# Optimization experiments

Hardware: AMD Instinct MI355X
Metric: run time of the kernel (lower is better)

## Reference

```python
import jax, jax.numpy as jnp
import numpy as np

D = 1024; H = 8; QLR = 384; KVLR = 256; NOPE = 128; ROPE = 64; VD = 128
E = 8; TOPK = 2; INTER = 512; NSH = 2; B = 2; T = 2048
QKD = NOPE + ROPE  # 192


def _rms(x, w, eps=1e-6):
    return x * jax.lax.rsqrt(jnp.mean(x * x, axis=-1, keepdims=True) + eps) * w


def _rope(x, cos, sin):
    # x: [B,T,h,ROPE]; pairs are consecutive elements (torch view(...,-1,2)).
    x0 = x[..., 0::2]
    x1 = x[..., 1::2]
    c = cos[None, :, None, :]
    s = sin[None, :, None, :]
    y0 = x0 * c - x1 * s
    y1 = x0 * s + x1 * c
    return jnp.stack([y0, y1], axis=-1).reshape(x.shape)


def setup_inputs() -> dict:
    key = jax.random.key(0)
    ks = jax.random.split(key, 12)
    def w(k, shape, scale=0.02):
        return jax.random.normal(k, shape, dtype=jnp.float32) * scale
    inv = 1.0 / (10000.0 ** (jnp.arange(0, ROPE, 2, dtype=jnp.float32) / ROPE))
    ang = jnp.arange(T, dtype=jnp.float32)[:, None] * inv[None, :]  # [T, ROPE//2]
    return {
        "x": jax.random.normal(ks[0], (B, T, D), dtype=jnp.float32),
        "freqs_cos": jnp.cos(ang),
        "freqs_sin": jnp.sin(ang),
        "rmsn1_w": jnp.ones((D,), jnp.float32),
        "rmsn2_w": jnp.ones((D,), jnp.float32),
        "latent_w": w(ks[1], (D, QLR + KVLR + ROPE)),
        "q_norm_w": jnp.ones((QLR,), jnp.float32),
        "q_up_w": w(ks[2], (QLR, H * QKD)),
        "kv_norm_w": jnp.ones((KVLR,), jnp.float32),
        "kv_up_w": w(ks[3], (KVLR, H * (NOPE + VD))),
        "c_proj_w": w(ks[4], (D, D)),
        "gate_w": w(ks[5], (D, E)),
        "sh_w1": w(ks[6], (D, INTER * NSH)),
        "sh_w2": w(ks[7], (INTER * NSH, D)),
        "sh_w3": w(ks[8], (D, INTER * NSH)),
        "e_w1": w(ks[9], (E, D, INTER)),
        "e_w2": w(ks[10], (E, INTER, D)),
        "e_w3": w(ks[11], (E, D, INTER)),
    }


def reference(x, freqs_cos, freqs_sin, rmsn1_w, rmsn2_w, latent_w, q_norm_w,
              q_up_w, kv_norm_w, kv_up_w, c_proj_w, gate_w, sh_w1, sh_w2,
              sh_w3, e_w1, e_w2, e_w3):
    Bx, Tx, _ = x.shape
    # ---- MLA attention ----
    h = _rms(x, rmsn1_w)
    lat = h @ latent_w
    q_l, kv_l, k_r = jnp.split(lat, [QLR, QLR + KVLR], axis=-1)
    q = (_rms(q_l, q_norm_w) @ q_up_w).reshape(Bx, Tx, H, QKD)
    q_n, q_r = q[..., :NOPE], q[..., NOPE:]
    q_r = _rope(q_r, freqs_cos, freqs_sin)
    q = jnp.concatenate([q_n, q_r], axis=-1)  # [B,T,H,QKD]
    kv = (_rms(kv_l, kv_norm_w) @ kv_up_w).reshape(Bx, Tx, H, NOPE + VD)
    k_n, v = kv[..., :NOPE], kv[..., NOPE:]
    k_r = _rope(k_r[:, :, None, :], freqs_cos, freqs_sin)
    k_r = jnp.broadcast_to(k_r, (Bx, Tx, H, ROPE))
    k = jnp.concatenate([k_n, k_r], axis=-1)
    scale = 1.0 / jnp.sqrt(jnp.float32(QKD))
    scores = jnp.einsum('bqhd,bkhd->bhqk', q, k) * scale
    causal = jnp.tril(jnp.ones((Tx, Tx), dtype=bool))
    scores = jnp.where(causal, scores, jnp.finfo(scores.dtype).min)
    attn = jax.nn.softmax(scores, axis=-1)
    y = jnp.einsum('bhqk,bkhd->bqhd', attn, v).reshape(Bx, Tx, D)
    x = x + y @ c_proj_w
    # ---- DeepSeekMoE ----
    h2 = _rms(x, rmsn2_w).reshape(-1, D)  # [N, D]
    y_sh = (jax.nn.silu(h2 @ sh_w1) * (h2 @ sh_w3)) @ sh_w2
    scores_g = jax.nn.softmax(h2 @ gate_w, axis=-1)  # [N, E]
    w_top, idx = jax.lax.top_k(scores_g, TOPK)  # weights == gathered original scores
    # combine weights per expert (route_scale = 1.0)
    cw = jnp.sum(jax.nn.one_hot(idx, E, dtype=h2.dtype) * w_top[..., None], axis=1)  # [N, E]
    h1 = jnp.einsum('nd,edi->eni', h2, e_w1)
    h3 = jnp.einsum('nd,edi->eni', h2, e_w3)
    out_e = jnp.einsum('eni,eid->end', jax.nn.silu(h1) * h3, e_w2)  # [E, N, D]
    y_moe = y_sh + jnp.einsum('end,ne->nd', out_e, cw)
    return x + y_moe.reshape(Bx, Tx, D)
```

## Files before the change

### kernel.cpp

```cpp
#include <hip/hip_runtime.h>
#include <hip/hip_bf16.h>
#include <math.h>

#define D_ 1024
#define H_ 8
#define QLR_ 384
#define KVLR_ 256
#define NOPE_ 128
#define ROPE_ 64
#define VD_ 128
#define E_ 8
#define INTER_ 512
#define B_ 2
#define T_ 2048
#define QKD_ 192
#define NTOK (B_*T_)
#define LSTR 4608
#define MAXMB 72

typedef __attribute__((ext_vector_type(8))) short short8;
typedef __attribute__((ext_vector_type(4))) float f32x4;
typedef __attribute__((ext_vector_type(4))) unsigned short us4;

__device__ __forceinline__ unsigned short f2bf(float f) {
  union { float f; unsigned u; } v; v.f = f;
  return (unsigned short)((v.u + 0x7FFFu + ((v.u >> 16) & 1u)) >> 16);
}
__device__ __forceinline__ float bf2f(unsigned short h) {
  union { unsigned u; float f; } v; v.u = ((unsigned)h) << 16;
  return v.f;
}

#define GLD16(SRC, DST) __builtin_amdgcn_global_load_lds( \
    (__attribute__((address_space(1))) void*)(SRC), \
    (__attribute__((address_space(3))) void*)(DST), 16, 0, 0)

#define DPPF(v, ctrl) __int_as_float(__builtin_amdgcn_update_dpp(0, __float_as_int(v), ctrl, 0xF, 0xF, true))
__device__ __forceinline__ float dppmax16(float v) {
  v = fmaxf(v, DPPF(v, 0xB1));
  v = fmaxf(v, DPPF(v, 0x4E));
  v = fmaxf(v, DPPF(v, 0x124));
  v = fmaxf(v, DPPF(v, 0x128));
  return v;
}
__device__ __forceinline__ float dppsum16(float v) {
  v += DPPF(v, 0xB1);
  v += DPPF(v, 0x4E);
  v += DPPF(v, 0x124);
  v += DPPF(v, 0x128);
  return v;
}

__device__ __forceinline__ void trans32(const float* __restrict__ src, unsigned short* __restrict__ dst,
                                        int R, int C, int c0, int r0, float (*tile)[33]) {
  int tx = threadIdx.x & 31, ty = threadIdx.x >> 5;
  #pragma unroll
  for (int i = 0; i < 4; ++i) {
    int rr = ty + i * 8;
    tile[rr][tx] = src[(size_t)(r0 + rr) * C + c0 + tx];
  }
  __syncthreads();
  #pragma unroll
  for (int i = 0; i < 4; ++i) {
    int rr = ty + i * 8;
    dst[(size_t)(c0 + rr) * R + r0 + tx] = f2bf(tile[tx][rr]);
  }
}
__device__ __forceinline__ void trans32p(const float* __restrict__ src, unsigned short* __restrict__ dst,
                                         int K, int C1, int c0, int r0, int f, float (*tile)[33]) {
  int tx = threadIdx.x & 31, ty = threadIdx.x >> 5;
  #pragma unroll
  for (int i = 0; i < 4; ++i) {
    int rr = ty + i * 8;
    tile[rr][tx] = src[(size_t)(r0 + rr) * C1 + c0 + tx];
  }
  __syncthreads();
  #pragma unroll
  for (int i = 0; i < 4; ++i) {
    int cc = ty + i * 8;
    int c = c0 + cc;
    int n = ((c >> 4) << 5) + (c & 15) + f;
    dst[(size_t)n * K + r0 + tx] = f2bf(tile[tx][cc]);
  }
}

__global__ __launch_bounds__(256) void prep1(
    const float* __restrict__ x, const float* __restrict__ rw, unsigned short* __restrict__ h_bf,
    const float* __restrict__ latent_w, unsigned short* __restrict__ Wlat) {
  __shared__ float tile[32][33];
  int b = blockIdx.x;
  if (b < NTOK) {
    int tid = threadIdx.x;
    const float* xr = x + (size_t)b * D_;
    float v[4]; float ss = 0.f;
    #pragma unroll
    for (int j = 0; j < 4; ++j) { v[j] = xr[tid + j * 256]; ss += v[j] * v[j]; }
    for (int o = 1; o < 64; o <<= 1) ss += __shfl_xor(ss, o);
    if ((tid & 63) == 0) tile[32][tid >> 6] = ss;
    __syncthreads();
    float inv = 1.f / sqrtf((tile[32][0] + tile[32][1] + tile[32][2] + tile[32][3]) / D_ + 1e-6f);
    #pragma unroll
    for (int j = 0; j < 4; ++j) {
      int i = tid + j * 256;
      h_bf[(size_t)b * D_ + i] = f2bf(v[j] * inv * rw[i]);
    }
    return;
  }
  b -= NTOK;
  trans32(latent_w, Wlat, 1024, 704, (b % 22) * 32, (b / 22) * 32, tile);
}

__global__ __launch_bounds__(256) void prep2(
    const unsigned short* __restrict__ h_bf, const unsigned short* __restrict__ Wlat,
    unsigned short* __restrict__ lat,
    const float* __restrict__ q_up_w, unsigned short* __restrict__ Wqup,
    const float* __restrict__ kv_up_w, unsigned short* __restrict__ Wkv,
    const float* __restrict__ c_proj_w, unsigned short* __restrict__ Wcp,
    const float* __restrict__ sh_w1, const float* __restrict__ sh_w3, unsigned short* __restrict__ Wsh13,
    const float* __restrict__ sh_w2, unsigned short* __restrict__ Wsh2,
    const float* __restrict__ e_w1, const float* __restrict__ e_w3, unsigned short* __restrict__ Wew13,
    const float* __restrict__ e_w2, unsigned short* __restrict__ Wew2) {
  __shared__ __align__(16) unsigned short As[128 * 32];
  __shared__ __align__(16) unsigned short Bs[128 * 32];
  __shared__ float tile[32][33];
  int b = blockIdx.x;
  if (b < 192) {
    const int tid = threadIdx.x, lane = tid & 63, wave = tid >> 6;
    const int wm = wave >> 1, wn = wave & 1;
    const int bm = (b / 6) * 128, bn = (b % 6) * 128;
    const int r = lane & 15, g = lane >> 4;
    f32x4 acc[4][4];
    #pragma unroll
    for (int i = 0; i < 4; ++i)
      #pragma unroll
      for (int j = 0; j < 4; ++j) acc[i][j] = (f32x4)0.f;
    const int rl0 = wave * 16 + (lane >> 2), rl1 = rl0 + 64;
    const int kc = (lane & 3) * 8;
    char* AsB = (char*)As; char* BsB = (char*)Bs;
    for (int k0 = 0; k0 < 1024; k0 += 32) {
      GLD16(h_bf + (size_t)(bm + rl0) * 1024 + k0 + kc, AsB + wave * 1024);
      GLD16(h_bf + (size_t)(bm + rl1) * 1024 + k0 + kc, AsB + (wave + 4) * 1024);
      GLD16(Wlat + (size_t)(bn + rl0) * 1024 + k0 + kc, BsB + wave * 1024);
      GLD16(Wlat + (size_t)(bn + rl1) * 1024 + k0 + kc, BsB + (wave + 4) * 1024);
      __syncthreads();
      short8 af[4], bfr[4];
      #pragma unroll
      for (int mi = 0; mi < 4; ++mi)
        af[mi] = *(const short8*)(As + (wm * 64 + mi * 16 + r) * 32 + g * 8);
      #pragma unroll
      for (int nj = 0; nj < 4; ++nj)
        bfr[nj] = *(const short8*)(Bs + (wn * 64 + nj * 16 + r) * 32 + g * 8);
      #pragma unroll
      for (int mi = 0; mi < 4; ++mi)
        #pragma unroll
        for (int nj = 0; nj < 4; ++nj)
          acc[mi][nj] = __builtin_amdgcn_mfma_f32_16x16x32_bf16(af[mi], bfr[nj], acc[mi][nj], 0, 0, 0);
      __syncthreads();
    }
    const int orow0 = wm * 64 + g * 4;
    const int ocol0 = bn + wn * 64 + r;
    #pragma unroll
    for (int mi = 0; mi < 4; ++mi)
      #pragma unroll
      for (int reg = 0; reg < 4; ++reg) {
        int mrow = bm + orow0 + mi * 16 + reg;
        size_t bas = (size_t)mrow * 768 + ocol0;
        #pragma unroll
        for (int nj = 0; nj < 4; ++nj) lat[bas + nj * 16] = f2bf(acc[mi][nj][reg]);
      }
    return;
  }
  b -= 192;
  if (b < 576) { trans32(q_up_w, Wqup, 384, 1536, (b % 48) * 32, (b / 48) * 32, tile); return; }
  b -= 576;
  if (b < 512) { trans32(kv_up_w, Wkv, 256, 2048, (b % 64) * 32, (b / 64) * 32, tile); return; }
  b -= 512;
  if (b < 1024) { trans32(c_proj_w, Wcp, 1024, 1024, (b % 32) * 32, (b / 32) * 32, tile); return; }
  b -= 1024;
  if (b < 1024) { trans32(sh_w2, Wsh2, 1024, 1024, (b % 32) * 32, (b / 32) * 32, tile); return; }
  b -= 1024;
  if (b < 2048) {
    int z = b / 1024, idx = b % 1024;
    trans32p(z ? sh_w3 : sh_w1, Wsh13, 1024, 1024, (idx % 32) * 32, (idx / 32) * 32, z * 16, tile);
    return;
  }
  b -= 2048;
  if (b < 8192) {
    int z = b / 512, idx = b % 512;
    int bat = z >> 1, f = (z & 1) * 16;
    const float* src = ((z & 1) ? e_w3 : e_w1) + (size_t)bat * 1024 * 512;
    trans32p(src, Wew13 + (size_t)bat * 1024 * 1024, 1024, 512, (idx % 16) * 32, (idx / 16) * 32, f, tile);
    return;
  }
  b -= 8192;
  {
    int z = b / 512, idx = b % 512;
    trans32(e_w2 + (size_t)z * 512 * 1024, Wew2 + (size_t)z * 1024 * 512,
            512, 1024, (idx % 32) * 32, (idx / 32) * 32, tile);
  }
}

__global__ __launch_bounds__(256) void lat_post(
    const unsigned short* __restrict__ lat, const float* __restrict__ qw,
    const float* __restrict__ kw, const float* __restrict__ fc, const float* __restrict__ fs,
    unsigned short* __restrict__ qn, unsigned short* __restrict__ kvn,
    unsigned short* __restrict__ kr) {
  int row = blockIdx.x, tid = threadIdx.x;
  int lane = tid & 63, wv = tid >> 6;
  const unsigned short* lr = lat + (size_t)row * 768;
  float s1 = 0.f, s2 = 0.f;
  for (int i = tid; i < QLR_; i += 256) { float v = bf2f(lr[i]); s1 += v * v; }
  { float v = bf2f(lr[QLR_ + tid]); s2 = v * v; }
  for (int o = 1; o < 64; o <<= 1) { s1 += __shfl_xor(s1, o); s2 += __shfl_xor(s2, o); }
  __shared__ float red[8];
  if (lane == 0) { red[wv] = s1; red[4 + wv] = s2; }
  __syncthreads();
  float inv1 = 1.f / sqrtf((red[0] + red[1] + red[2] + red[3]) / QLR_ + 1e-6f);
  float inv2 = 1.f / sqrtf((red[4] + red[5] + red[6] + red[7]) / KVLR_ + 1e-6f);
  for (int i = tid; i < QLR_; i += 256)
    qn[(size_t)row * QLR_ + i] = f2bf(bf2f(lr[i]) * inv1 * qw[i]);
  kvn[(size_t)row * KVLR_ + tid] = f2bf(bf2f(lr[QLR_ + tid]) * inv2 * kw[tid]);
  if (tid < 32) {
    int t = row & (T_ - 1);
    float c = fc[t * 32 + tid], s = fs[t * 32 + tid];
    float x0 = bf2f(lr[640 + 2 * tid]), x1 = bf2f(lr[640 + 2 * tid + 1]);
    kr[(size_t)row * ROPE_ + 2 * tid]     = f2bf(x0 * c - x1 * s);
    kr[(size_t)row * ROPE_ + 2 * tid + 1] = f2bf(x0 * s + x1 * c);
  }
}

template<int MODE>
__global__ __launch_bounds__(256) void gemm_bf16(
    const unsigned short* __restrict__ A, const unsigned short* __restrict__ Bt,
    void* __restrict__ Cv, int M, int N, int K,
    const float* __restrict__ addv) {
  __shared__ __align__(16) unsigned short As[128 * 32];
  __shared__ __align__(16) unsigned short Bs[128 * 32];
  const int tid = threadIdx.x;
  const int lane = tid & 63, wave = tid >> 6;
  const int wm = wave >> 1, wn = wave & 1;
  const int bm = blockIdx.y * 128, bn = blockIdx.x * 128;
  const int r = lane & 15, g = lane >> 4;

  f32x4 acc[4][4];
  #pragma unroll
  for (int i = 0; i < 4; ++i)
    #pragma unroll
    for (int j = 0; j < 4; ++j) acc[i][j] = (f32x4)0.f;

  const int rl0 = wave * 16 + (lane >> 2);
  const int rl1 = rl0 + 64;
  const int kc = (lane & 3) * 8;
  char* AsB = (char*)As; char* BsB = (char*)Bs;

  for (int k0 = 0; k0 < K; k0 += 32) {
    GLD16(A + (size_t)(bm + rl0) * K + k0 + kc, AsB + wave * 1024);
    GLD16(A + (size_t)(bm + rl1) * K + k0 + kc, AsB + (wave + 4) * 1024);
    GLD16(Bt + (size_t)(bn + rl0) * K + k0 + kc, BsB + wave * 1024);
    GLD16(Bt + (size_t)(bn + rl1) * K + k0 + kc, BsB + (wave + 4) * 1024);
    __syncthreads();
    short8 af[4], bfr[4];
    #pragma unroll
    for (int mi = 0; mi < 4; ++mi)
      af[mi] = *(const short8*)(As + (wm * 64 + mi * 16 + r) * 32 + g * 8);
    #pragma unroll
    for (int nj = 0; nj < 4; ++nj)
      bfr[nj] = *(const short8*)(Bs + (wn * 64 + nj * 16 + r) * 32 + g * 8);
    #pragma unroll
    for (int mi = 0; mi < 4; ++mi)
      #pragma unroll
      for (int nj = 0; nj < 4; ++nj)
        acc[mi][nj] = __builtin_amdgcn_mfma_f32_16x16x32_bf16(af[mi], bfr[nj], acc[mi][nj], 0, 0, 0);
    __syncthreads();
  }

  const int orow0 = wm * 64 + g * 4;
  const int ocol0 = bn + wn * 64 + r;
  #pragma unroll
  for (int mi = 0; mi < 4; ++mi) {
    #pragma unroll
    for (int reg = 0; reg < 4; ++reg) {
      int mrow = bm + orow0 + mi * 16 + reg;
      size_t bas = (size_t)mrow * N + ocol0;
      if (MODE == 0) {
        unsigned short* C = (unsigned short*)Cv;
        #pragma unroll
        for (int nj = 0; nj < 4; ++nj) C[bas + nj * 16] = f2bf(acc[mi][nj][reg]);
      } else {
        float* C = (float*)Cv;
        #pragma unroll
        for (int nj = 0; nj < 4; ++nj) C[bas + nj * 16] = acc[mi][nj][reg] + addv[bas + nj * 16];
      }
    }
  }
}

__global__ __launch_bounds__(256) void gemm_qkv(
    const unsigned short* __restrict__ qn, const unsigned short* __restrict__ Wqup,
    const unsigned short* __restrict__ kvn, const unsigned short* __restrict__ Wkv,
    unsigned short* __restrict__ qq, unsigned short* __restrict__ kvb,
    unsigned short* __restrict__ vtg) {
  __shared__ __align__(16) unsigned short As[128 * 32];
  __shared__ __align__(16) unsigned short Bs[128 * 32];
  const int tid = threadIdx.x;
  const int lane = tid & 63, wave = tid >> 6;
  const int wm = wave >> 1, wn = wave & 1;
  const bool isQ = blockIdx.x < 12;
  const int bx = isQ ? blockIdx.x : blockIdx.x - 12;
  const unsigned short* A  = isQ ? qn : kvn;
  const unsigned short* Bt = isQ ? Wqup : Wkv;
  const int K = isQ ? QLR_ : KVLR_;
  const int bm = blockIdx.y * 128, bn = bx * 128;
  const int r = lane & 15, g = lane >> 4;

  f32x4 acc[4][4];
  #pragma unroll
  for (int i = 0; i < 4; ++i)
    #pragma unroll
    for (int j = 0; j < 4; ++j) acc[i][j] = (f32x4)0.f;

  const int rl0 = wave * 16 + (lane >> 2);
  const int rl1 = rl0 + 64;
  const int kc = (lane & 3) * 8;
  char* AsB = (char*)As; char* BsB = (char*)Bs;

  for (int k0 = 0; k0 < K; k0 += 32) {
    GLD16(A + (size_t)(bm + rl0) * K + k0 + kc, AsB + wave * 1024);
    GLD16(A + (size_t)(bm + rl1) * K + k0 + kc, AsB + (wave + 4) * 1024);
    GLD16(Bt + (size_t)(bn + rl0) * K + k0 + kc, BsB + wave * 1024);
    GLD16(Bt + (size_t)(bn + rl1) * K + k0 + kc, BsB + (wave + 4) * 1024);
    __syncthreads();
    short8 af[4], bfr[4];
    #pragma unroll
    for (int mi = 0; mi < 4; ++mi)
      af[mi] = *(const short8*)(As + (wm * 64 + mi * 16 + r) * 32 + g * 8);
    #pragma unroll
    for (int nj = 0; nj < 4; ++nj)
      bfr[nj] = *(const short8*)(Bs + (wn * 64 + nj * 16 + r) * 32 + g * 8);
    #pragma unroll
    for (int mi = 0; mi < 4; ++mi)
      #pragma unroll
      for (int nj = 0; nj < 4; ++nj)
        acc[mi][nj] = __builtin_amdgcn_mfma_f32_16x16x32_bf16(af[mi], bfr[nj], acc[mi][nj], 0, 0, 0);
    __syncthreads();
  }

  if (isQ) {
    const int orow0 = wm * 64 + g * 4;
    const int ocol0 = bn + wn * 64 + r;
    #pragma unroll
    for (int mi = 0; mi < 4; ++mi)
      #pragma unroll
      for (int reg = 0; reg < 4; ++reg) {
        int mrow = bm + orow0 + mi * 16 + reg;
        size_t bas = (size_t)mrow * 1536 + ocol0;
        #pragma unroll
        for (int nj = 0; nj < 4; ++nj) qq[bas + nj * 16] = f2bf(acc[mi][nj][reg]);
      }
  } else {
    const int colbase = bn + wn * 64;
    const int b = bm >> 11;
    const int hh = colbase >> 8;
    if ((colbase & 255) < 128) {
      #pragma unroll
      for (int mi = 0; mi < 4; ++mi)
        #pragma unroll
        for (int reg = 0; reg < 4; ++reg) {
          int mrow = bm + wm * 64 + mi * 16 + g * 4 + reg;
          size_t bas = (size_t)mrow * 2048 + colbase + r;
          #pragma unroll
          for (int nj = 0; nj < 4; ++nj) kvb[bas + nj * 16] = f2bf(acc[mi][nj][reg]);
        }
    } else {
      const int tl0 = (bm & 2047) + wm * 64 + g * 4;
      const int d0 = (colbase & 255) - 128 + r;
      const size_t bhbase = (size_t)(b * 8 + hh) * 64;
      #pragma unroll
      for (int mi = 0; mi < 4; ++mi) {
        int t = tl0 + mi * 16;
        size_t tb = (bhbase + (t >> 5)) * 4096 + (t & 31);
        #pragma unroll
        for (int nj = 0; nj < 4; ++nj) {
          int d = d0 + nj * 16;
          us4 pk;
          #pragma unroll
          for (int reg = 0; reg < 4; ++reg) pk[reg] = f2bf(acc[mi][nj][reg]);
          *(us4*)(vtg + tb + (size_t)d * 32) = pk;
        }
      }
    }
  }
}

__global__ __launch_bounds__(256) void gemm_ffn13(
    const unsigned short* __restrict__ h2b, const unsigned short* __restrict__ Wsh13,
    unsigned short* __restrict__ t1m,
    const unsigned short* __restrict__ Wew13, unsigned short* __restrict__ ehm,
    const int* __restrict__ lists, const int* __restrict__ map, const int* __restrict__ sbase) {
  __shared__ __align__(16) unsigned short As[128 * 32];
  __shared__ __align__(16) unsigned short Bs[128 * 32];
  const int i = blockIdx.x;
  const bool isSh = i < 512;
  const int tid = threadIdx.x, lane = tid & 63, wave = tid >> 6;
  const int wm = wave >> 1, wn = wave & 1;
  const int r = lane & 15, g = lane >> 4;
  const int rl0 = wave * 16 + (lane >> 2), rl1 = rl0 + 64;
  const int kc = (lane & 3) * 8;

  int bn, e = 0, ib = 0, bm = 0;
  const unsigned short* Bt;
  int ar0, ar1;
  const unsigned short* A;
  if (isSh) {
    bn = (i & 15) * 128; bm = (i >> 4) * 128;
    Bt = Wsh13; A = h2b;
    ar0 = bm + rl0; ar1 = bm + rl1;
  } else {
    int j = i - 512;
    bn = (j & 7) * 128;
    int mb = map[j >> 3];
    if (mb < 0) return;
    e = mb >> 16; ib = mb & 0xFFFF;
    Bt = Wew13 + (size_t)e * 1024 * 1024; A = h2b;
    ar0 = lists[e * LSTR + ib * 128 + rl0]; if (ar0 < 0) ar0 = 0;
    ar1 = lists[e * LSTR + ib * 128 + rl1]; if (ar1 < 0) ar1 = 0;
  }

  f32x4 acc[4][4];
  #pragma unroll
  for (int a = 0; a < 4; ++a)
    #pragma unroll
    for (int bj = 0; bj < 4; ++bj) acc[a][bj] = (f32x4)0.f;
  char* AsB = (char*)As; char* BsB = (char*)Bs;

  for (int k0 = 0; k0 < 1024; k0 += 32) {
    GLD16(A + (size_t)ar0 * 1024 + k0 + kc, AsB + wave * 1024);
    GLD16(A + (size_t)ar1 * 1024 + k0 + kc, AsB + (wave + 4) * 1024);
    GLD16(Bt + (size_t)(bn + rl0) * 1024 + k0 + kc, BsB + wave * 1024);
    GLD16(Bt + (size_t)(bn + rl1) * 1024 + k0 + kc, BsB + (wave + 4) * 1024);
    __syncthreads();
    short8 af[4], bfr[4];
    #pragma unroll
    for (int mi = 0; mi < 4; ++mi)
      af[mi] = *(const short8*)(As + (wm * 64 + mi * 16 + r) * 32 + g * 8);
    #pragma unroll
    for (int nj = 0; nj < 4; ++nj)
      bfr[nj] = *(const short8*)(Bs + (wn * 64 + nj * 16 + r) * 32 + g * 8);
    #pragma unroll
    for (int mi = 0; mi < 4; ++mi)
      #pragma unroll
      for (int nj = 0; nj < 4; ++nj)
        acc[mi][nj] = __builtin_amdgcn_mfma_f32_16x16x32_bf16(af[mi], bfr[nj], acc[mi][nj], 0, 0, 0);
    __syncthreads();
  }

  if (isSh) {
    const int hc = ((bn + wn * 64) >> 1) + r;
    #pragma unroll
    for (int mi = 0; mi < 4; ++mi)
      #pragma unroll
      for (int reg = 0; reg < 4; ++reg) {
        int mrow = bm + wm * 64 + mi * 16 + g * 4 + reg;
        #pragma unroll
        for (int p = 0; p < 2; ++p) {
          float a = acc[mi][2 * p][reg], b3 = acc[mi][2 * p + 1][reg];
          t1m[(size_t)mrow * 1024 + hc + p * 16] = f2bf((a / (1.f + __expf(-a))) * b3);
        }
      }
  } else {
    const int sb = sbase[e] + ib * 128;
    const int hc = ((bn + wn * 64) >> 1) + r;
    #pragma unroll
    for (int mi = 0; mi < 4; ++mi)
      #pragma unroll
      for (int reg = 0; reg < 4; ++reg) {
        int srow = sb + wm * 64 + mi * 16 + g * 4 + reg;
        #pragma unroll
        for (int p = 0; p < 2; ++p) {
          float a = acc[mi][2 * p][reg], b3 = acc[mi][2 * p + 1][reg];
          ehm[(size_t)srow * 512 + hc + p * 16] = f2bf((a / (1.f + __expf(-a))) * b3);
        }
      }
  }
}

__global__ __launch_bounds__(256) void gemm_ffn2(
    const unsigned short* __restrict__ t1m, const unsigned short* __restrict__ Wsh2,
    const unsigned short* __restrict__ ehm, const unsigned short* __restrict__ Wew2,
    float* __restrict__ out,
    const int* __restrict__ lists, const int* __restrict__ map, const int* __restrict__ sbase,
    const float* __restrict__ cw) {
  __shared__ __align__(16) unsigned short As[128 * 32];
  __shared__ __align__(16) unsigned short Bs[128 * 32];
  const int i = blockIdx.x;
  const bool isSh = i < 256;
  const int tid = threadIdx.x, lane = tid & 63, wave = tid >> 6;
  const int wm = wave >> 1, wn = wave & 1;
  const int r = lane & 15, g = lane >> 4;
  const int rl0 = wave * 16 + (lane >> 2), rl1 = rl0 + 64;
  const int kc = (lane & 3) * 8;

  int bn, e = 0, ib = 0, bm = 0, K;
  const unsigned short* A;
  const unsigned short* Bt;
  if (isSh) {
    bn = (i & 7) * 128; bm = (i >> 3) * 128;
    A = t1m; Bt = Wsh2; K = 1024;
  } else {
    int j = i - 256;
    bn = (j & 7) * 128;
    int mb = map[j >> 3];
    if (mb < 0) return;
    e = mb >> 16; ib = mb & 0xFFFF;
    bm = sbase[e] + ib * 128;
    A = ehm; Bt = Wew2 + (size_t)e * 512 * 1024; K = 512;
  }

  f32x4 acc[4][4];
  #pragma unroll
  for (int a = 0; a < 4; ++a)
    #pragma unroll
    for (int bj = 0; bj < 4; ++bj) acc[a][bj] = (f32x4)0.f;
  char* AsB = (char*)As; char* BsB = (char*)Bs;

  for (int k0 = 0; k0 < K; k0 += 32) {
    GLD16(A + (size_t)(bm + rl0) * K + k0 + kc, AsB + wave * 1024);
    GLD16(A + (size_t)(bm + rl1) * K + k0 + kc, AsB + (wave + 4) * 1024);
    GLD16(Bt + (size_t)(bn + rl0) * K + k0 + kc, BsB + wave * 1024);
    GLD16(Bt + (size_t)(bn + rl1) * K + k0 + kc, BsB + (wave + 4) * 1024);
    __syncthreads();
    short8 af[4], bfr[4];
    #pragma unroll
    for (int mi = 0; mi < 4; ++mi)
      af[mi] = *(const short8*)(As + (wm * 64 + mi * 16 + r) * 32 + g * 8);
    #pragma unroll
    for (int nj = 0; nj < 4; ++nj)
      bfr[nj] = *(const short8*)(Bs + (wn * 64 + nj * 16 + r) * 32 + g * 8);
    #pragma unroll
    for (int mi = 0; mi < 4; ++mi)
      #pragma unroll
      for (int nj = 0; nj < 4; ++nj)
        acc[mi][nj] = __builtin_amdgcn_mfma_f32_16x16x32_bf16(af[mi], bfr[nj], acc[mi][nj], 0, 0, 0);
    __syncthreads();
  }

  const int ocol0 = bn + wn * 64 + r;
  if (isSh) {
    #pragma unroll
    for (int mi = 0; mi < 4; ++mi)
      #pragma unroll
      for (int reg = 0; reg < 4; ++reg) {
        int mrow = bm + wm * 64 + mi * 16 + g * 4 + reg;
        #pragma unroll
        for (int nj = 0; nj < 4; ++nj)
          atomicAdd(out + (size_t)mrow * 1024 + ocol0 + nj * 16, acc[mi][nj][reg]);
      }
  } else {
    #pragma unroll
    for (int mi = 0; mi < 4; ++mi)
      #pragma unroll
      for (int reg = 0; reg < 4; ++reg) {
        int orow = wm * 64 + mi * 16 + g * 4 + reg;
        int tok = lists[e * LSTR + ib * 128 + orow];
        if (tok >= 0) {
          float wt = cw[(size_t)tok * E_ + e];
          #pragma unroll
          for (int nj = 0; nj < 4; ++nj)
            atomicAdd(out + (size_t)tok * 1024 + ocol0 + nj * 16, acc[mi][nj][reg] * wt);
        }
      }
  }
}

#define AQ 128
#define AK 32
#define VP 40
__global__ __launch_bounds__(512) void attn_mfma(
    const unsigned short* __restrict__ q,
    const unsigned short* __restrict__ kv,
    const unsigned short* __restrict__ kr,
    const unsigned short* __restrict__ vt,
    const float* __restrict__ fcos, const float* __restrict__ fsin,
    unsigned short* __restrict__ po,
    float* __restrict__ pml) {
  __shared__ __align__(16) unsigned short Ks[AK * 192];
  __shared__ __align__(16) unsigned short Vl[128 * VP];
  __shared__ __align__(16) unsigned short Ps[8 * 16 * VP];
  const int tid = threadIdx.x, lane = tid & 63, wave = tid >> 6;
  const int r = lane & 15, g = lane >> 4;
  const int bh = blockIdx.y, b = bh >> 3, h = bh & 7;
  const int qt = gridDim.x - 1 - blockIdx.x;
  const int q0 = qt * AQ;
  const int half = blockIdx.z;
  const int hnt = 2 * (qt + 1);
  const int kb = half * hnt, ke = kb + hnt;
  const size_t bT = (size_t)b * T_;
  const unsigned short* vbase = vt + (size_t)bh * 64 * 4096;
  char* KsB = (char*)Ks;

  short8 qf[6];
  const int qrow = q0 + wave * 16 + r;
  {
    const unsigned short* qb = q + ((bT + qrow) * H_ + h) * 192;
    #pragma unroll
    for (int kk = 0; kk < 6; ++kk) qf[kk] = *(const short8*)(qb + kk * 32 + g * 8);
    #pragma unroll
    for (int kk = 4; kk < 6; ++kk) {
      int i0 = (kk - 4) * 16 + g * 4;
      #pragma unroll
      for (int p = 0; p < 4; ++p) {
        float cc = fcos[qrow * 32 + i0 + p], sn = fsin[qrow * 32 + i0 + p];
        float x0 = bf2f((unsigned short)qf[kk][2 * p]), x1 = bf2f((unsigned short)qf[kk][2 * p + 1]);
        qf[kk][2 * p]     = (short)f2bf(x0 * cc - x1 * sn);
        qf[kk][2 * p + 1] = (short)f2bf(x0 * sn + x1 * cc);
      }
    }
  }

  float m_i[4], l_i[4];
  f32x4 o[8];
  #pragma unroll
  for (int i = 0; i < 4; ++i) { m_i[i] = -1e30f; l_i[i] = 0.f; }
  #pragma unroll
  for (int cb = 0; cb < 8; ++cb) o[cb] = (f32x4)0.f;

  const float scale2 = 0.07216878364870322f * 1.44269504088896f;

  const int kr0r = tid / 24, kr0c = tid % 24;
  const bool k1v = tid < 256;
  const int kr1r = (tid + 512) / 24, kr1c = (tid + 512) % 24;

  short8 kreg0, kreg1, vreg;
  {
    int kk0 = kb * AK;
    kreg0 = (kr0c < 16)
      ? *(const short8*)(kv + ((bT + kk0 + kr0r) * H_ + h) * 256 + kr0c * 8)
      : *(const short8*)(kr + (bT + kk0 + kr0r) * 64 + (kr0c - 16) * 8);
    if (k1v)
      kreg1 = (kr1c < 16)
        ? *(const short8*)(kv + ((bT + kk0 + kr1r) * H_ + h) * 256 + kr1c * 8)
        : *(const short8*)(kr + (bT + kk0 + kr1r) * 64 + (kr1c - 16) * 8);
    vreg = *(const short8*)(vbase + (size_t)kb * 4096 + tid * 8);
  }

  for (int kt = kb; kt < ke; ++kt) {
    __builtin_amdgcn_s_barrier();
    __builtin_amdgcn_sched_barrier(0);
    *(short8*)(KsB + ((kr0r * 384 + kr0c * 16) ^ ((kr0r & 7) << 4))) = kreg0;
    if (k1v)
      *(short8*)(KsB + ((kr1r * 384 + kr1c * 16) ^ ((kr1r & 7) << 4))) = kreg1;
    *(short8*)(Vl + (tid >> 2) * VP + (tid & 3) * 8) = vreg;
    asm volatile("s_waitcnt lgkmcnt(0)" ::: "memory");
    __builtin_amdgcn_s_barrier();
    __builtin_amdgcn_sched_barrier(0);

    if (kt + 1 < ke) {
      int k1 = (kt + 1) * AK;
      kreg0 = (kr0c < 16)
        ? *(const short8*)(kv + ((bT + k1 + kr0r) * H_ + h) * 256 + kr0c * 8)
        : *(const short8*)(kr + (bT + k1 + kr0r) * 64 + (kr0c - 16) * 8);
      if (k1v)
        kreg1 = (kr1c < 16)
          ? *(const short8*)(kv + ((bT + k1 + kr1r) * H_ + h) * 256 + kr1c * 8)
          : *(const short8*)(kr + (bT + k1 + kr1r) * 64 + (kr1c - 16) * 8);
      vreg = *(const short8*)(vbase + (size_t)(kt + 1) * 4096 + tid * 8);
    }

    const int k0 = kt * AK;
    f32x4 sf0 = (f32x4)0.f, sf1 = (f32x4)0.f;
    {
      int ksw = (r & 7) << 4;
      __builtin_amdgcn_s_setprio(1);
      #pragma unroll
      for (int kk = 0; kk < 6; ++kk) {
        short8 b0 = *(const short8*)(KsB + ((r * 384 + kk * 64 + g * 16) ^ ksw));
        short8 b1 = *(const short8*)(KsB + (((16 + r) * 384 + kk * 64 + g * 16) ^ ksw));
        sf0 = __builtin_amdgcn_mfma_f32_16x16x32_bf16(qf[kk], b0, sf0, 0, 0, 0);
        sf1 = __builtin_amdgcn_mfma_f32_16x16x32_bf16(qf[kk], b1, sf1, 0, 0, 0);
      }
      __builtin_amdgcn_s_setprio(0);
    }

    float fac[4];
    bool needs = false;
    const bool bnd = (k0 + AK > q0);
    #pragma unroll
    for (int reg = 0; reg < 4; ++reg) {
      float s0 = sf0[reg] * scale2;
      float s1 = sf1[reg] * scale2;
      if (bnd) {
        int qp = q0 + wave * 16 + g * 4 + reg;
        if (k0 + r > qp) s0 = -1e30f;
        if (k0 + 16 + r > qp) s1 = -1e30f;
      }
      float mt = dppmax16(fmaxf(s0, s1));
      float fc = 1.f, mn = m_i[reg];
      if (mt > mn + 8.f) {
        mn = mt; fc = exp2f(m_i[reg] - mn); m_i[reg] = mn; needs = true;
      }
      float e0 = exp2f(s0 - mn), e1 = exp2f(s1 - mn);
      float rs = dppsum16(e0 + e1);
      l_i[reg] = l_i[reg] * fc + rs;
      fac[reg] = fc;
      __hip_bfloat162 pk = __float22bfloat162_rn(float2{e0, e1});
      unsigned u = *(unsigned*)&pk;
      int prow = g * 4 + reg;
      Ps[wave * 16 * VP + prow * VP + r] = (unsigned short)u;
      Ps[wave * 16 * VP + prow * VP + 16 + r] = (unsigned short)(u >> 16);
    }
    if (__any(needs)) {
      #pragma unroll
      for (int cb = 0; cb < 8; ++cb)
        #pragma unroll
        for (int reg = 0; reg < 4; ++reg) o[cb][reg] *= fac[reg];
    }
    short8 pa = *(const short8*)(Ps + wave * 16 * VP + r * VP + g * 8);
    __builtin_amdgcn_s_setprio(1);
    #pragma unroll
    for (int cb = 0; cb < 8; ++cb) {
      short8 vb = *(const short8*)(Vl + (cb * 16 + r) * VP + g * 8);
      o[cb] = __builtin_amdgcn_mfma_f32_16x16x32_bf16(pa, vb, o[cb], 0, 0, 0);
    }
    __builtin_amdgcn_s_setprio(0);
  }

  const int slab = (bh * 16 + qt) * 2 + half;
  unsigned short* pob = po + (size_t)slab * 16384;
  float* pmlb = pml + (size_t)slab * 256;
  #pragma unroll
  for (int reg = 0; reg < 4; ++reg) {
    int row = wave * 16 + g * 4 + reg;
    if (r == 0) { pmlb[row * 2] = m_i[reg]; pmlb[row * 2 + 1] = l_i[reg]; }
    #pragma unroll
    for (int cb = 0; cb < 8; ++cb)
      pob[row * 128 + cb * 16 + r] = f2bf(o[cb][reg]);
  }
}

__global__ __launch_bounds__(512) void attn_combine(
    const unsigned short* __restrict__ po, const float* __restrict__ pml,
    unsigned short* __restrict__ y) {
  const int qt = blockIdx.x, bh = blockIdx.y, b = bh >> 3, h = bh & 7;
  const int s0 = (bh * 16 + qt) * 2, s1 = s0 + 1;
  const int row = threadIdx.x >> 2;
  const int qp = threadIdx.x & 3;
  float m0 = pml[(size_t)s0 * 256 + row * 2], l0 = pml[(size_t)s0 * 256 + row * 2 + 1];
  float m1 = pml[(size_t)s1 * 256 + row * 2], l1 = pml[(size_t)s1 * 256 + row * 2 + 1];
  float m = fmaxf(m0, m1);
  float e0 = exp2f(m0 - m), e1 = exp2f(m1 - m);
  float inv = 1.f / (l0 * e0 + l1 * e1);
  e0 *= inv; e1 *= inv;
  const unsigned short* o0 = po + (size_t)s0 * 16384 + row * 128 + qp * 32;
  const unsigned short* o1 = po + (size_t)s1 * 16384 + row * 128 + qp * 32;
  unsigned short* yb = y + ((size_t)(b * T_ + qt * 128 + row)) * 1024 + h * 128 + qp * 32;
  #pragma unroll
  for (int v = 0; v < 4; ++v) {
    short8 a = *(const short8*)(o0 + v * 8);
    short8 c = *(const short8*)(o1 + v * 8);
    short8 w;
    #pragma unroll
    for (int j = 0; j < 8; ++j)
      w[j] = (short)f2bf(bf2f((unsigned short)a[j]) * e0 + bf2f((unsigned short)c[j]) * e1);
    *(short8*)(yb + v * 8) = w;
  }
}

__global__ __launch_bounds__(256) void rms2_gate(
    const float* __restrict__ xo, const float* __restrict__ rw, const float* __restrict__ gw,
    unsigned short* __restrict__ h2b, float* __restrict__ cw) {
  int row = blockIdx.x, tid = threadIdx.x;
  int lane = tid & 63, wv = tid >> 6;
  const float* xr = xo + (size_t)row * D_;
  float v[4]; float ss = 0.f;
  #pragma unroll
  for (int j = 0; j < 4; ++j) { v[j] = xr[tid + j * 256]; ss += v[j] * v[j]; }
  for (int o = 1; o < 64; o <<= 1) ss += __shfl_xor(ss, o);
  __shared__ float red[4];
  if (lane == 0) red[wv] = ss;
  __syncthreads();
  float inv = 1.f / sqrtf((red[0] + red[1] + red[2] + red[3]) / D_ + 1e-6f);
  float a[E_] = {0, 0, 0, 0, 0, 0, 0, 0};
  #pragma unroll
  for (int j = 0; j < 4; ++j) {
    int i = tid + j * 256;
    float hv = v[j] * inv * rw[i];
    h2b[(size_t)row * D_ + i] = f2bf(hv);
    const float* wr = gw + (size_t)i * E_;
    #pragma unroll
    for (int e = 0; e < E_; ++e) a[e] += hv * wr[e];
  }
  #pragma unroll
  for (int e = 0; e < E_; ++e) {
    float t = a[e];
    for (int o = 1; o < 64; o <<= 1) t += __shfl_xor(t, o);
    a[e] = t;
  }
  __shared__ float ga[4][E_];
  if (lane == 0)
    #pragma unroll
    for (int e = 0; e < E_; ++e) ga[wv][e] = a[e];
  __syncthreads();
  if (tid == 0) {
    float lg[E_];
    #pragma unroll
    for (int e = 0; e < E_; ++e) lg[e] = ga[0][e] + ga[1][e] + ga[2][e] + ga[3][e];
    float mx = lg[0];
    #pragma unroll
    for (int e = 1; e < E_; ++e) mx = fmaxf(mx, lg[e]);
    float sum = 0.f; float p[E_];
    #pragma unroll
    for (int e = 0; e < E_; ++e) { p[e] = __expf(lg[e] - mx); sum += p[e]; }
    float is = 1.f / sum;
    int i1 = 0; float b1 = p[0];
    #pragma unroll
    for (int e = 1; e < E_; ++e) if (p[e] > b1) { b1 = p[e]; i1 = e; }
    int i2 = -1; float b2 = -1.f;
    #pragma unroll
    for (int e = 0; e < E_; ++e) if (e != i1 && p[e] > b2) { b2 = p[e]; i2 = e; }
    #pragma unroll
    for (int e = 0; e < E_; ++e)
      cw[(size_t)row * E_ + e] = (e == i1) ? b1 * is : (e == i2 ? b2 * is : 0.f);
  }
}

__global__ __launch_bounds__(256) void moe_build(const float* __restrict__ cw,
                                                 int* __restrict__ lists, int* __restrict__ counts) {
  int e = blockIdx.x, tid = threadIdx.x;
  int lane = tid & 63, wv = tid >> 6;
  __shared__ int wsum[4];
  __shared__ int base;
  if (tid == 0) base = 0;
  __syncthreads();
  for (int c0 = 0; c0 < NTOK; c0 += 256) {
    int tok = c0 + tid;
    bool f = cw[(size_t)tok * E_ + e] > 0.f;
    unsigned long long m = __ballot(f);
    int pos = __popcll(m & ((1ull << lane) - 1ull));
    if (lane == 0) wsum[wv] = __popcll(m);
    __syncthreads();
    int woff = base;
    #pragma unroll
    for (int w = 0; w < 4; ++w) if (w < wv) woff += wsum[w];
    if (f) lists[e * LSTR + woff + pos] = tok;
    __syncthreads();
    if (tid == 0) base += wsum[0] + wsum[1] + wsum[2] + wsum[3];
    __syncthreads();
  }
  int cnt = base;
  int padded = (cnt + 127) & ~127;
  for (int i2 = cnt + tid; i2 < padded; i2 += 256) lists[e * LSTR + i2] = -1;
  if (tid == 0) { counts[e] = cnt; counts[8 + e] = padded >> 7; }
}

__global__ void moe_finalize(const int* __restrict__ counts, int* __restrict__ map,
                             int* __restrict__ sbase) {
  if (threadIdx.x == 0 && blockIdx.x == 0) {
    int cum = 0;
    for (int e = 0; e < E_; ++e) {
      sbase[e] = cum * 128;
      int nb = counts[8 + e];
      for (int i = 0; i < nb; ++i) map[cum + i] = (e << 16) | i;
      cum += nb;
    }
    for (; cum < MAXMB; ++cum) map[cum] = -1;
  }
}

extern "C" void kernel_launch(void* const* d_in, const int* in_sizes, int n_in,
                              void* d_out, int out_size, void* d_ws, size_t ws_size,
                              hipStream_t stream) {
  const float* x        = (const float*)d_in[0];
  const float* fcos     = (const float*)d_in[1];
  const float* fsin     = (const float*)d_in[2];
  const float* rmsn1_w  = (const float*)d_in[3];
  const float* rmsn2_w  = (const float*)d_in[4];
  const float* latent_w = (const float*)d_in[5];
  const float* q_norm_w = (const float*)d_in[6];
  const float* q_up_w   = (const float*)d_in[7];
  const float* kv_norm_w= (const float*)d_in[8];
  const float* kv_up_w  = (const float*)d_in[9];
  const float* c_proj_w = (const float*)d_in[10];
  const float* gate_w   = (const float*)d_in[11];
  const float* sh_w1    = (const float*)d_in[12];
  const float* sh_w2    = (const float*)d_in[13];
  const float* sh_w3    = (const float*)d_in[14];
  const float* e_w1     = (const float*)d_in[15];
  const float* e_w2     = (const float*)d_in[16];
  const float* e_w3     = (const float*)d_in[17];
  float* out = (float*)d_out;

  char* base = (char*)d_ws;
  size_t off = 0;
  auto take = [&](size_t bytes) { char* p = base + off; off += (bytes + 255) & ~(size_t)255; return p; };
  unsigned short* Wlat  = (unsigned short*)take((size_t)768 * 1024 * 2);
  unsigned short* Wqup  = (unsigned short*)take((size_t)1536 * 384 * 2);
  unsigned short* Wkv   = (unsigned short*)take((size_t)2048 * 256 * 2);
  unsigned short* Wcp   = (unsigned short*)take((size_t)1024 * 1024 * 2);
  unsigned short* Wsh13 = (unsigned short*)take((size_t)2048 * 1024 * 2);
  unsigned short* Wsh2  = (unsigned short*)take((size_t)1024 * 1024 * 2);
  unsigned short* Wew13 = (unsigned short*)take((size_t)8 * 1024 * 1024 * 2);
  unsigned short* Wew2  = (unsigned short*)take((size_t)8 * 1024 * 512 * 2);
  float* cw             = (float*)take((size_t)NTOK * E_ * 4);
  int* lists            = (int*)take((size_t)E_ * LSTR * 4);
  int* counts           = (int*)take(64 * 4);
  int* map              = (int*)take(MAXMB * 4);
  int* sbase            = (int*)take(E_ * 4);
  unsigned short* Vtg   = (unsigned short*)take((size_t)16 * 64 * 4096 * 2);
  unsigned short* kr    = (unsigned short*)take((size_t)NTOK * 64 * 2);
  float* pml            = (float*)take((size_t)512 * 256 * 4);

  size_t actStart = off;
  size_t aoff = actStart;
  auto takeA = [&](size_t bytes) { char* p = base + aoff; aoff += (bytes + 255) & ~(size_t)255; return p; };
  unsigned short* h_bf = (unsigned short*)takeA((size_t)NTOK * 1024 * 2);
  unsigned short* lat  = (unsigned short*)takeA((size_t)NTOK * 768 * 2);
  unsigned short* qn   = (unsigned short*)takeA((size_t)NTOK * 384 * 2);
  unsigned short* kvn  = (unsigned short*)takeA((size_t)NTOK * 256 * 2);
  unsigned short* qq   = (unsigned short*)takeA((size_t)NTOK * 1536 * 2);
  unsigned short* kvb  = (unsigned short*)takeA((size_t)NTOK * 2048 * 2);
  unsigned short* y    = (unsigned short*)takeA((size_t)NTOK * 1024 * 2);

  unsigned short* po   = (unsigned short*)(base + actStart);

  size_t coff = actStart;
  auto takeC = [&](size_t bytes) { char* p = base + coff; coff += (bytes + 255) & ~(size_t)255; return p; };
  unsigned short* h2b  = (unsigned short*)takeC((size_t)NTOK * 1024 * 2);
  unsigned short* t1m  = (unsigned short*)takeC((size_t)NTOK * 1024 * 2);
  unsigned short* ehm  = (unsigned short*)takeC((size_t)9216 * 512 * 2);

  dim3 blk(256);

  prep1<<<dim3(NTOK + 704), blk, 0, stream>>>(x, rmsn1_w, h_bf, latent_w, Wlat);
  prep2<<<dim3(192 + 576 + 512 + 1024 + 1024 + 2048 + 8192 + 4096), blk, 0, stream>>>(
      h_bf, Wlat, lat, q_up_w, Wqup, kv_up_w, Wkv, c_proj_w, Wcp,
      sh_w1, sh_w3, Wsh13, sh_w2, Wsh2, e_w1, e_w3, Wew13, e_w2, Wew2);
  lat_post<<<NTOK, blk, 0, stream>>>(lat, q_norm_w, kv_norm_w, fcos, fsin, qn, kvn, kr);
  gemm_qkv<<<dim3(28, 32), blk, 0, stream>>>(qn, Wqup, kvn, Wkv, qq, kvb, Vtg);
  attn_mfma<<<dim3(T_ / AQ, B_ * H_, 2), dim3(512), 0, stream>>>(qq, kvb, kr, Vtg, fcos, fsin, po, pml);
  attn_combine<<<dim3(T_ / AQ, B_ * H_), dim3(512), 0, stream>>>(po, pml, y);
  gemm_bf16<1><<<dim3(8, 32), blk, 0, stream>>>(y, Wcp, out, NTOK, 1024, 1024, x);
  rms2_gate<<<NTOK, blk, 0, stream>>>(out, rmsn2_w, gate_w, h2b, cw);
  moe_build<<<E_, blk, 0, stream>>>(cw, lists, counts);
  moe_finalize<<<1, 64, 0, stream>>>(counts, map, sbase);
  gemm_ffn13<<<dim3(1088), blk, 0, stream>>>(h2b, Wsh13, t1m, Wew13, ehm, lists, map, sbase);
  gemm_ffn2<<<dim3(832), blk, 0, stream>>>(t1m, Wsh2, ehm, Wew2, out, lists, map, sbase, cw);
}
```

Baseline: 359.7 us.

## Split causal attention KV range into fixed-size chunks and compact K-nope buffer

```diff
diff --git a/kernel.cpp b/kernel.cpp
--- a/kernel.cpp
+++ b/kernel.cpp
@@ -367,7 +367,7 @@
         #pragma unroll
         for (int reg = 0; reg < 4; ++reg) {
           int mrow = bm + wm * 64 + mi * 16 + g * 4 + reg;
-          size_t bas = (size_t)mrow * 2048 + colbase + r;
+          size_t bas = (size_t)mrow * 1024 + hh * 128 + (colbase & 255) + r;
           #pragma unroll
           for (int nj = 0; nj < 4; ++nj) kvb[bas + nj * 16] = f2bf(acc[mi][nj][reg]);
         }
@@ -589,11 +589,16 @@
   const int tid = threadIdx.x, lane = tid & 63, wave = tid >> 6;
   const int r = lane & 15, g = lane >> 4;
   const int bh = blockIdx.y, b = bh >> 3, h = bh & 7;
-  const int qt = gridDim.x - 1 - blockIdx.x;
+  const int Stab[17] = {0,1,2,3,4,6,8,10,12,15,18,21,24,28,32,36,40};
+  const int cid = 39 - (int)blockIdx.x;
+  int qt = 0;
+  #pragma unroll
+  for (int t = 1; t <= 15; ++t) if (cid >= Stab[t]) qt = t;
+  const int chunk = cid - Stab[qt];
   const int q0 = qt * AQ;
-  const int half = blockIdx.z;
-  const int hnt = 2 * (qt + 1);
-  const int kb = half * hnt, ke = kb + hnt;
+  const int ntl = 4 * (qt + 1);
+  const int kb = chunk * 16;
+  const int ke = (kb + 16 < ntl) ? kb + 16 : ntl;
   const size_t bT = (size_t)b * T_;
   const unsigned short* vbase = vt + (size_t)bh * 64 * 4096;
   char* KsB = (char*)Ks;
@@ -634,11 +639,11 @@
   {
     int kk0 = kb * AK;
     kreg0 = (kr0c < 16)
-      ? *(const short8*)(kv + ((bT + kk0 + kr0r) * H_ + h) * 256 + kr0c * 8)
+      ? *(const short8*)(kv + ((bT + kk0 + kr0r) * H_ + h) * 128 + kr0c * 8)
       : *(const short8*)(kr + (bT + kk0 + kr0r) * 64 + (kr0c - 16) * 8);
     if (k1v)
       kreg1 = (kr1c < 16)
-        ? *(const short8*)(kv + ((bT + kk0 + kr1r) * H_ + h) * 256 + kr1c * 8)
+        ? *(const short8*)(kv + ((bT + kk0 + kr1r) * H_ + h) * 128 + kr1c * 8)
         : *(const short8*)(kr + (bT + kk0 + kr1r) * 64 + (kr1c - 16) * 8);
     vreg = *(const short8*)(vbase + (size_t)kb * 4096 + tid * 8);
   }
@@ -657,11 +662,11 @@
     if (kt + 1 < ke) {
       int k1 = (kt + 1) * AK;
       kreg0 = (kr0c < 16)
-        ? *(const short8*)(kv + ((bT + k1 + kr0r) * H_ + h) * 256 + kr0c * 8)
+        ? *(const short8*)(kv + ((bT + k1 + kr0r) * H_ + h) * 128 + kr0c * 8)
         : *(const short8*)(kr + (bT + k1 + kr0r) * 64 + (kr0c - 16) * 8);
       if (k1v)
         kreg1 = (kr1c < 16)
-          ? *(const short8*)(kv + ((bT + k1 + kr1r) * H_ + h) * 256 + kr1c * 8)
+          ? *(const short8*)(kv + ((bT + k1 + kr1r) * H_ + h) * 128 + kr1c * 8)
           : *(const short8*)(kr + (bT + k1 + kr1r) * 64 + (kr1c - 16) * 8);
       vreg = *(const short8*)(vbase + (size_t)(kt + 1) * 4096 + tid * 8);
     }
@@ -724,7 +729,7 @@
     __builtin_amdgcn_s_setprio(0);
   }
 
-  const int slab = (bh * 16 + qt) * 2 + half;
+  const int slab = bh * 40 + cid;
   unsigned short* pob = po + (size_t)slab * 16384;
   float* pmlb = pml + (size_t)slab * 256;
   #pragma unroll
@@ -741,27 +746,42 @@
     const unsigned short* __restrict__ po, const float* __restrict__ pml,
     unsigned short* __restrict__ y) {
   const int qt = blockIdx.x, bh = blockIdx.y, b = bh >> 3, h = bh & 7;
-  const int s0 = (bh * 16 + qt) * 2, s1 = s0 + 1;
+  const int Stab[17] = {0,1,2,3,4,6,8,10,12,15,18,21,24,28,32,36,40};
+  const int s0 = bh * 40 + Stab[qt];
+  const int nc = Stab[qt + 1] - Stab[qt];
   const int row = threadIdx.x >> 2;
   const int qp = threadIdx.x & 3;
-  float m0 = pml[(size_t)s0 * 256 + row * 2], l0 = pml[(size_t)s0 * 256 + row * 2 + 1];
-  float m1 = pml[(size_t)s1 * 256 + row * 2], l1 = pml[(size_t)s1 * 256 + row * 2 + 1];
-  float m = fmaxf(m0, m1);
-  float e0 = exp2f(m0 - m), e1 = exp2f(m1 - m);
-  float inv = 1.f / (l0 * e0 + l1 * e1);
-  e0 *= inv; e1 *= inv;
-  const unsigned short* o0 = po + (size_t)s0 * 16384 + row * 128 + qp * 32;
-  const unsigned short* o1 = po + (size_t)s1 * 16384 + row * 128 + qp * 32;
+  float mj[4], lj[4];
+  float m = -1e30f;
+  for (int j = 0; j < nc; ++j) {
+    mj[j] = pml[(size_t)(s0 + j) * 256 + row * 2];
+    lj[j] = pml[(size_t)(s0 + j) * 256 + row * 2 + 1];
+    m = fmaxf(m, mj[j]);
+  }
+  float lsum = 0.f;
+  float ej[4];
+  for (int j = 0; j < nc; ++j) {
+    ej[j] = exp2f(mj[j] - m);
+    lsum += lj[j] * ej[j];
+  }
+  float inv = 1.f / lsum;
   unsigned short* yb = y + ((size_t)(b * T_ + qt * 128 + row)) * 1024 + h * 128 + qp * 32;
   #pragma unroll
   for (int v = 0; v < 4; ++v) {
-    short8 a = *(const short8*)(o0 + v * 8);
-    short8 c = *(const short8*)(o1 + v * 8);
-    short8 w;
-    #pragma unroll
-    for (int j = 0; j < 8; ++j)
-      w[j] = (short)f2bf(bf2f((unsigned short)a[j]) * e0 + bf2f((unsigned short)c[j]) * e1);
-    *(short8*)(yb + v * 8) = w;
+    float accv[8];
+    #pragma unroll
+    for (int jj = 0; jj < 8; ++jj) accv[jj] = 0.f;
+    for (int j = 0; j < nc; ++j) {
+      const unsigned short* oj = po + (size_t)(s0 + j) * 16384 + row * 128 + qp * 32 + v * 8;
+      short8 a = *(const short8*)oj;
+      float w = ej[j];
+      #pragma unroll
+      for (int jj = 0; jj < 8; ++jj) accv[jj] += bf2f((unsigned short)a[jj]) * w;
+    }
+    short8 wv;
+    #pragma unroll
+    for (int jj = 0; jj < 8; ++jj) wv[jj] = (short)f2bf(accv[jj] * inv);
+    *(short8*)(yb + v * 8) = wv;
   }
 }
 
@@ -907,7 +927,6 @@
   int* sbase            = (int*)take(E_ * 4);
   unsigned short* Vtg   = (unsigned short*)take((size_t)16 * 64 * 4096 * 2);
   unsigned short* kr    = (unsigned short*)take((size_t)NTOK * 64 * 2);
-  float* pml            = (float*)take((size_t)512 * 256 * 4);
 
   size_t actStart = off;
   size_t aoff = actStart;
@@ -917,10 +936,10 @@
   unsigned short* qn   = (unsigned short*)takeA((size_t)NTOK * 384 * 2);
   unsigned short* kvn  = (unsigned short*)takeA((size_t)NTOK * 256 * 2);
   unsigned short* qq   = (unsigned short*)takeA((size_t)NTOK * 1536 * 2);
-  unsigned short* kvb  = (unsigned short*)takeA((size_t)NTOK * 2048 * 2);
+  unsigned short* kvb  = (unsigned short*)takeA((size_t)NTOK * 1024 * 2);
   unsigned short* y    = (unsigned short*)takeA((size_t)NTOK * 1024 * 2);
-
-  unsigned short* po   = (unsigned short*)(base + actStart);
+  unsigned short* po   = (unsigned short*)takeA((size_t)640 * 16384 * 2);
+  float* pml           = (float*)takeA((size_t)640 * 256 * 4);
 
   size_t coff = actStart;
   auto takeC = [&](size_t bytes) { char* p = base + coff; coff += (bytes + 255) & ~(size_t)255; return p; };
@@ -936,8 +955,8 @@
       sh_w1, sh_w3, Wsh13, sh_w2, Wsh2, e_w1, e_w3, Wew13, e_w2, Wew2);
   lat_post<<<NTOK, blk, 0, stream>>>(lat, q_norm_w, kv_norm_w, fcos, fsin, qn, kvn, kr);
   gemm_qkv<<<dim3(28, 32), blk, 0, stream>>>(qn, Wqup, kvn, Wkv, qq, kvb, Vtg);
-  attn_mfma<<<dim3(T_ / AQ, B_ * H_, 2), dim3(512), 0, stream>>>(qq, kvb, kr, Vtg, fcos, fsin, po, pml);
-  attn_combine<<<dim3(T_ / AQ, B_ * H_), dim3(512), 0, stream>>>(po, pml, y);
+  attn_mfma<<<dim3(40, 16), dim3(512), 0, stream>>>(qq, kvb, kr, Vtg, fcos, fsin, po, pml);
+  attn_combine<<<dim3(16, 16), dim3(512), 0, stream>>>(po, pml, y);
   gemm_bf16<1><<<dim3(8, 32), blk, 0, stream>>>(y, Wcp, out, NTOK, 1024, 1024, x);
   rms2_gate<<<NTOK, blk, 0, stream>>>(out, rmsn2_w, gate_w, h2b, cw);
   moe_build<<<E_, blk, 0, stream>>>(cw, lists, counts);
```

Measured after the change: 344.9 us. -4.1%, faster.
